# Optimization experiments

Measured on AMD Instinct MI355X. Metric: run time of the kernel, lower is better.

## Reference

```python
import jax, jax.numpy as jnp
import numpy as np

N_NODES = 50000
N_EDGES = 1600000
EMB = 128
HID = 128
OUT = 128
HEADS = 4
BN_EPS = 1e-5


def segment_softmax(e, seg, n):
    # numerically-stable softmax over variable-degree neighborhoods
    m = jax.ops.segment_max(e, seg, num_segments=n)
    m = jnp.where(jnp.isfinite(m), m, 0.0)
    ex = jnp.exp(e - m[seg])
    s = jax.ops.segment_sum(ex, seg, num_segments=n)
    return ex / (s[seg] + 1e-16)


def gat_layer(x, src, dst, W, att_src, att_dst, bias, concat):
    # PyG GATConv (eval mode, self-loops already added to src/dst)
    N = x.shape[0]
    H, C = att_src.shape
    h = (x @ W).reshape(N, H, C)                       # [N,H,C]
    a_src = jnp.einsum('nhc,hc->nh', h, att_src)       # [N,H]
    a_dst = jnp.einsum('nhc,hc->nh', h, att_dst)
    e = jax.nn.leaky_relu(a_src[src] + a_dst[dst], 0.2)  # [E,H]
    alpha = segment_softmax(e, dst, N)                 # [E,H]
    out = jax.ops.segment_sum(h[src] * alpha[:, :, None], dst, num_segments=N)
    out = out.reshape(N, H * C) if concat else out.mean(axis=1)
    return out + bias


def setup_inputs() -> dict:
    key = jax.random.key(0)
    ks = jax.random.split(key, 16)
    C1 = HID // HEADS
    inp = {
        'node_embeddings': jax.random.normal(ks[0], (N_NODES, EMB), jnp.float32),
        'edge_index': jax.random.randint(ks[1], (2, N_EDGES), 0, N_NODES, jnp.int64),
        'proj_W': jax.random.normal(ks[2], (EMB, HID), jnp.float32) * 0.05,
        'proj_b': jnp.zeros((HID,), jnp.float32),
        'W1': jax.random.normal(ks[3], (HID, HEADS * C1), jnp.float32) * 0.05,
        'att_src1': jax.random.normal(ks[4], (HEADS, C1), jnp.float32) * 0.05,
        'att_dst1': jax.random.normal(ks[5], (HEADS, C1), jnp.float32) * 0.05,
        'bias1': jnp.zeros((HEADS * C1,), jnp.float32),
        'bn_gamma': jnp.ones((HID,), jnp.float32),
        'bn_beta': jnp.zeros((HID,), jnp.float32),
        'W2': jax.random.normal(ks[6], (HID, HEADS * OUT), jnp.float32) * 0.05,
        'att_src2': jax.random.normal(ks[7], (HEADS, OUT), jnp.float32) * 0.05,
        'att_dst2': jax.random.normal(ks[8], (HEADS, OUT), jnp.float32) * 0.05,
        'bias2': jnp.zeros((OUT,), jnp.float32),
        'out_W': jax.random.normal(ks[9], (OUT, OUT), jnp.float32) * 0.05,
        'out_b': jnp.zeros((OUT,), jnp.float32),
    }
    return inp


def reference(node_embeddings, edge_index, proj_W, proj_b,
              W1, att_src1, att_dst1, bias1, bn_gamma, bn_beta,
              W2, att_src2, att_dst2, bias2, out_W, out_b):
    N = node_embeddings.shape[0]
    # add self-loops (PyG GATConv default)
    loops = jnp.arange(N, dtype=edge_index.dtype)
    src = jnp.concatenate([edge_index[0], loops])
    dst = jnp.concatenate([edge_index[1], loops])

    x = jax.nn.relu(node_embeddings @ proj_W + proj_b)
    x = gat_layer(x, src, dst, W1, att_src1, att_dst1, bias1, concat=True)
    # BatchNorm1d in eval mode: running_mean=0, running_var=1
    x = x / jnp.sqrt(1.0 + BN_EPS) * bn_gamma + bn_beta
    x = jax.nn.elu(x)
    # dropout is identity in eval mode
    x = gat_layer(x, src, dst, W2, att_src2, att_dst2, bias2, concat=False)
    x = x.mean(axis=0, keepdims=True)                  # [1, OUT]
    x = jax.nn.relu(x @ out_W + out_b)
    return x
```

## Files before the change

### kernel.cpp

```cpp
#include <hip/hip_runtime.h>
#include <hip/hip_bf16.h>

#define NN 50000
#define NROW 50048
#define NE 1600000
#define ETOT (NE + NN)
#define BN_K 0.9999950000374997f

#define SHIFT 7
#define NPB 128
#define NB ((NN + NPB - 1) >> SHIFT)
#define CAP 5120
#define CHUNK 4096
#define PGRID ((ETOT + CHUNK - 1) / CHUNK)
#define CVB (NROW * 32 / 256)

typedef __bf16 bf16x8 __attribute__((ext_vector_type(8)));
typedef float f32x4 __attribute__((ext_vector_type(4)));

__device__ __forceinline__ float leaky02(float x) { return x > 0.f ? x : 0.2f * x; }

__device__ __forceinline__ unsigned short f2bf(float f) {
    unsigned int u = __float_as_uint(f);
    u += 0x7FFFu + ((u >> 16) & 1u);
    return (unsigned short)(u >> 16);
}

__global__ void init_k(int* __restrict__ bcur_d, int* __restrict__ bcur_s,
                       float* __restrict__ y) {
    int t = threadIdx.x;
    if (t < NB) { bcur_d[t] = t * CAP; bcur_s[t] = t * CAP; }
    y[t] = 0.f;
}

__global__ void cvtw_k(const float* __restrict__ x0, unsigned short* __restrict__ x0b,
                       const float* __restrict__ pW, const float* __restrict__ W1,
                       unsigned short* __restrict__ pWt, unsigned short* __restrict__ W1t,
                       const float* __restrict__ W2, const float* __restrict__ as2,
                       const float* __restrict__ ad2, float* __restrict__ va_s,
                       float* __restrict__ va_d) {
    int b = blockIdx.x;
    if (b < CVB) {
        int g = b * 256 + threadIdx.x;
        int row = g >> 5;
        float4 v = make_float4(0.f, 0.f, 0.f, 0.f);
        if (row < NN) v = *(const float4*)&x0[(long)g * 4];
        ushort4 u;
        u.x = f2bf(v.x); u.y = f2bf(v.y); u.z = f2bf(v.z); u.w = f2bf(v.w);
        *(ushort4*)&x0b[(long)g * 4] = u;
    } else if (b < CVB + 2) {
        const float* in = (b - CVB) ? W1 : pW;
        unsigned short* outp = (b - CVB) ? W1t : pWt;
        for (int i = threadIdx.x; i < 16384; i += 256) {
            int n = i & 127, k = i >> 7;
            outp[n * 128 + k] = f2bf(in[k * 128 + n]);
        }
    } else {
        int h = b - CVB - 2;
        int k = threadIdx.x;
        if (k < 128) {
            const float* wrow = W2 + (long)k * 512 + h * 128;
            float accs = 0.f, accd = 0.f;
            for (int ci = 0; ci < 128; ++ci) {
                float w = wrow[ci];
                accs += w * as2[h * 128 + ci];
                accd += w * ad2[h * 128 + ci];
            }
            va_s[h * 128 + k] = accs;
            va_d[h * 128 + k] = accd;
        }
    }
}

__global__ __launch_bounds__(256) void fgemm_k(
    const unsigned short* __restrict__ x0b, const unsigned short* __restrict__ pWt,
    const unsigned short* __restrict__ W1t, const float* __restrict__ pb,
    const float* __restrict__ attS, const float* __restrict__ attD,
    unsigned short* __restrict__ h1b, float* __restrict__ aS, float* __restrict__ aD) {
    __shared__ unsigned short x1s[128][136];
    const int tid = threadIdx.x;
    const int wv = tid >> 6, l = tid & 63;
    const int lr = l & 15, lg = l >> 4;
    const int r0 = blockIdx.x * 128;
    const int wr = wv * 32;

    bf16x8 Af[2][4];
    f32x4 acc[2][8];

    #pragma unroll
    for (int rt = 0; rt < 2; ++rt)
        #pragma unroll
        for (int kt = 0; kt < 4; ++kt)
            Af[rt][kt] = *(const bf16x8*)&x0b[(long)(r0 + wr + rt * 16 + lr) * 128 + kt * 32 + lg * 8];
    #pragma unroll
    for (int rt = 0; rt < 2; ++rt)
        #pragma unroll
        for (int ct = 0; ct < 8; ++ct)
            acc[rt][ct] = (f32x4){0.f, 0.f, 0.f, 0.f};
    #pragma unroll
    for (int ct = 0; ct < 8; ++ct) {
        bf16x8 Bf[4];
        #pragma unroll
        for (int kt = 0; kt < 4; ++kt)
            Bf[kt] = *(const bf16x8*)&pWt[(ct * 16 + lr) * 128 + kt * 32 + lg * 8];
        #pragma unroll
        for (int kt = 0; kt < 4; ++kt) {
            acc[0][ct] = __builtin_amdgcn_mfma_f32_16x16x32_bf16(Af[0][kt], Bf[kt], acc[0][ct], 0, 0, 0);
            acc[1][ct] = __builtin_amdgcn_mfma_f32_16x16x32_bf16(Af[1][kt], Bf[kt], acc[1][ct], 0, 0, 0);
        }
    }
    #pragma unroll
    for (int ct = 0; ct < 8; ++ct) {
        int col = ct * 16 + lr;
        float bv = pb[col];
        #pragma unroll
        for (int rt = 0; rt < 2; ++rt)
            #pragma unroll
            for (int r = 0; r < 4; ++r) {
                float v = acc[rt][ct][r] + bv;
                x1s[wr + rt * 16 + lg * 4 + r][col] = f2bf(v > 0.f ? v : 0.f);
            }
    }
    __syncthreads();

    #pragma unroll
    for (int rt = 0; rt < 2; ++rt)
        #pragma unroll
        for (int kt = 0; kt < 4; ++kt)
            Af[rt][kt] = *(const bf16x8*)&x1s[wr + rt * 16 + lr][kt * 32 + lg * 8];
    #pragma unroll
    for (int rt = 0; rt < 2; ++rt)
        #pragma unroll
        for (int ct = 0; ct < 8; ++ct)
            acc[rt][ct] = (f32x4){0.f, 0.f, 0.f, 0.f};
    #pragma unroll
    for (int ct = 0; ct < 8; ++ct) {
        bf16x8 Bf[4];
        #pragma unroll
        for (int kt = 0; kt < 4; ++kt)
            Bf[kt] = *(const bf16x8*)&W1t[(ct * 16 + lr) * 128 + kt * 32 + lg * 8];
        #pragma unroll
        for (int kt = 0; kt < 4; ++kt) {
            acc[0][ct] = __builtin_amdgcn_mfma_f32_16x16x32_bf16(Af[0][kt], Bf[kt], acc[0][ct], 0, 0, 0);
            acc[1][ct] = __builtin_amdgcn_mfma_f32_16x16x32_bf16(Af[1][kt], Bf[kt], acc[1][ct], 0, 0, 0);
        }
    }
    __syncthreads();
    #pragma unroll
    for (int ct = 0; ct < 8; ++ct)
        #pragma unroll
        for (int rt = 0; rt < 2; ++rt)
            #pragma unroll
            for (int r = 0; r < 4; ++r)
                x1s[wr + rt * 16 + lg * 4 + r][ct * 16 + lr] = f2bf(acc[rt][ct][r]);
    __syncthreads();

    #pragma unroll
    for (int i = 0; i < 8; ++i) {
        int idx = tid + i * 256;
        int row = idx >> 4, cc = idx & 15;
        bf16x8 hv = *(const bf16x8*)&x1s[row][cc * 8];
        *(bf16x8*)&h1b[(long)(r0 + row) * 128 + cc * 8] = hv;
        int head = cc >> 2, lc = (cc & 3) * 8;
        float ps = 0.f, pd = 0.f;
        #pragma unroll
        for (int j = 0; j < 8; ++j) {
            float v = (float)hv[j];
            ps += v * attS[head * 32 + lc + j];
            pd += v * attD[head * 32 + lc + j];
        }
        ps += __shfl_xor(ps, 1); ps += __shfl_xor(ps, 2);
        pd += __shfl_xor(pd, 1); pd += __shfl_xor(pd, 2);
        if ((cc & 3) == 0) {
            aS[(r0 + row) * 4 + head] = ps;
            aD[(r0 + row) * 4 + head] = pd;
        }
    }
}

__global__ __launch_bounds__(512) void part_k(const int* __restrict__ srcA,
                                              const int* __restrict__ dstA,
                                              int* __restrict__ bcur_d, int* __restrict__ bcur_s,
                                              int* __restrict__ pr_d, int* __restrict__ pr_s) {
    __shared__ int cnt[NB], gb[NB], lo[NB];
    __shared__ int scanbuf[512];
    __shared__ int stg[CHUNK];
    __shared__ int dbuf[CHUNK];
    int t = threadIdx.x;
    int e0 = blockIdx.x * CHUNK;
    int e1 = min(e0 + CHUNK, ETOT);
    #pragma unroll
    for (int it = 0; it < 2; ++it) {
        int* bcur = it ? bcur_s : bcur_d;
        int* pr   = it ? pr_s   : pr_d;
        for (int i = t; i < NB; i += 512) cnt[i] = 0;
        __syncthreads();
        for (int e = e0 + t; e < e1; e += 512) {
            int s, d;
            if (e < NE) { s = srcA[e]; d = dstA[e]; } else { s = d = e - NE; }
            atomicAdd(&cnt[(it ? s : d) >> SHIFT], 1);
        }
        __syncthreads();
        for (int i = t; i < NB; i += 512)
            if (cnt[i]) gb[i] = atomicAdd(&bcur[i], cnt[i]);
        scanbuf[t] = (t < NB) ? cnt[t] : 0;
        __syncthreads();
        for (int dd = 1; dd < 512; dd <<= 1) {
            int y = (t >= dd) ? scanbuf[t - dd] : 0;
            __syncthreads();
            scanbuf[t] += y;
            __syncthreads();
        }
        if (t < NB) lo[t] = scanbuf[t] - cnt[t];
        __syncthreads();
        if (t < NB) cnt[t] = lo[t];
        __syncthreads();
        for (int e = e0 + t; e < e1; e += 512) {
            int s, d;
            if (e < NE) { s = srcA[e]; d = dstA[e]; } else { s = d = e - NE; }
            int n = it ? s : d, pay = it ? d : s;
            int key = n >> SHIFT;
            int idx = atomicAdd(&cnt[key], 1);
            stg[idx]  = ((n & (NPB - 1)) << 16) | pay;
            dbuf[idx] = gb[key] + (idx - lo[key]);
        }
        __syncthreads();
        int tot = e1 - e0;
        for (int p = t; p < tot; p += 512)
            pr[dbuf[p]] = stg[p];
        __syncthreads();
    }
}

__global__ void fine_k(const int* __restrict__ pr_d, const int* __restrict__ bcur_d,
                       int2* __restrict__ oe_d, int* __restrict__ csr_src,
                       const int* __restrict__ pr_s, const int* __restrict__ bcur_s,
                       int2* __restrict__ oe_s, int* __restrict__ csr_dst) {
    bool dk = blockIdx.x < NB;
    const int* pr    = dk ? pr_d : pr_s;
    const int* bcurb = dk ? bcur_d : bcur_s;
    int2* oe         = dk ? oe_d : oe_s;
    int* csr         = dk ? csr_src : csr_dst;
    int bkt = dk ? blockIdx.x : blockIdx.x - NB;
    __shared__ int cnt[NPB], off[NPB];
    int n0 = bkt << SHIFT;
    int base = bkt * CAP, end = bcurb[bkt];
    int t = threadIdx.x;
    if (t < NPB) cnt[t] = 0;
    __syncthreads();
    for (int i = base + t; i < end; i += 256)
        atomicAdd(&cnt[pr[i] >> 16], 1);
    __syncthreads();
    if (t < NPB) off[t] = cnt[t];
    __syncthreads();
    for (int dd = 1; dd < NPB; dd <<= 1) {
        int y = 0;
        if (t < NPB && t >= dd) y = off[t - dd];
        __syncthreads();
        if (t < NPB) off[t] += y;
        __syncthreads();
    }
    if (t < NPB) {
        int excl = off[t] - cnt[t];
        int n = n0 + t;
        if (n < NN) oe[n] = make_int2(base + excl, cnt[t]);
        off[t] = excl;
        cnt[t] = 0;
    }
    __syncthreads();
    for (int i = base + t; i < end; i += 256) {
        int p = pr[i];
        int j = p >> 16;
        int pos = base + off[j] + atomicAdd(&cnt[j], 1);
        csr[pos] = p & 0xFFFF;
    }
}

__global__ void gather1_k(const int* __restrict__ csr_src, const int2* __restrict__ oe_d,
                          const float* __restrict__ aS, const float* __restrict__ aD,
                          const unsigned short* __restrict__ h1b, const float* __restrict__ b1,
                          const float* __restrict__ bg, const float* __restrict__ bb,
                          const float* __restrict__ va_s, const float* __restrict__ va_d,
                          unsigned short* __restrict__ x2b, float* __restrict__ aS2,
                          float* __restrict__ aD2) {
    __shared__ float4 wst[4][64];
    __shared__ unsigned sst[4][64];
    int wv = threadIdx.x >> 6;
    int d = (blockIdx.x << 2) + wv;
    if (d >= NN) return;
    int lane = threadIdx.x & 63;
    float4 ad4 = *(const float4*)&aD[d * 4];
    int2 oe = oe_d[d];
    int o0 = oe.x, deg = oe.y, o1 = o0 + deg;

    float s0 = 0.f, s1 = 0.f, s2 = 0.f, s3 = 0.f;
    for (int base = o0; base < o1; base += 64) {
        int e = base + lane;
        if (e < o1) {
            int s = csr_src[e];
            float4 as4 = *(const float4*)&aS[s * 4];
            float4 w;
            w.x = __expf(leaky02(as4.x + ad4.x));
            w.y = __expf(leaky02(as4.y + ad4.y));
            w.z = __expf(leaky02(as4.z + ad4.z));
            w.w = __expf(leaky02(as4.w + ad4.w));
            wst[wv][lane] = w;
            sst[wv][lane] = (unsigned)(s << 8);
            s0 += w.x; s1 += w.y; s2 += w.z; s3 += w.w;
        }
    }
    #pragma unroll
    for (int off = 32; off; off >>= 1) {
        s0 += __shfl_xor(s0, off);
        s1 += __shfl_xor(s1, off);
        s2 += __shfl_xor(s2, off);
        s3 += __shfl_xor(s3, off);
    }
    float i0 = 1.f / (s0 + 1e-16f), i1 = 1.f / (s1 + 1e-16f);
    float i2 = 1.f / (s2 + 1e-16f), i3 = 1.f / (s3 + 1e-16f);

    int k = lane & 31, half = lane >> 5;
    unsigned cb = (unsigned)(k * 8);
    int headk = k >> 3;
    const char* h1base = (const char*)h1b;
    float a0 = 0.f, a1 = 0.f, a2 = 0.f, a3 = 0.f;

    if (deg <= 64) {
        if (lane < deg) {
            float4 w = wst[wv][lane];
            w.x *= i0; w.y *= i1; w.z *= i2; w.w *= i3;
            wst[wv][lane] = w;
        }
        __threadfence_block();
        for (int t = half; t < deg; t += 2) {
            float w = ((const float*)&wst[wv][t])[headk];
            unsigned ro = sst[wv][t];
            uint2 hv = *(const uint2*)(h1base + ro + cb);
            a0 += w * __uint_as_float(hv.x << 16);
            a1 += w * __uint_as_float(hv.x & 0xFFFF0000u);
            a2 += w * __uint_as_float(hv.y << 16);
            a3 += w * __uint_as_float(hv.y & 0xFFFF0000u);
        }
    } else {
        for (int base = o0; base < o1; base += 64) {
            int e = base + lane;
            if (e < o1) {
                int s = csr_src[e];
                float4 as4 = *(const float4*)&aS[s * 4];
                float4 w;
                w.x = __expf(leaky02(as4.x + ad4.x)) * i0;
                w.y = __expf(leaky02(as4.y + ad4.y)) * i1;
                w.z = __expf(leaky02(as4.z + ad4.z)) * i2;
                w.w = __expf(leaky02(as4.w + ad4.w)) * i3;
                wst[wv][lane] = w;
                sst[wv][lane] = (unsigned)(s << 8);
            }
            __threadfence_block();
            int nst = min(64, o1 - base);
            for (int t = half; t < nst; t += 2) {
                float w = ((const float*)&wst[wv][t])[headk];
                unsigned ro = sst[wv][t];
                uint2 hv = *(const uint2*)(h1base + ro + cb);
                a0 += w * __uint_as_float(hv.x << 16);
                a1 += w * __uint_as_float(hv.x & 0xFFFF0000u);
                a2 += w * __uint_as_float(hv.y << 16);
                a3 += w * __uint_as_float(hv.y & 0xFFFF0000u);
            }
            __threadfence_block();
        }
    }
    a0 += __shfl_xor(a0, 32); a1 += __shfl_xor(a1, 32);
    a2 += __shfl_xor(a2, 32); a3 += __shfl_xor(a3, 32);

    int c = k * 4;
    float v0 = (a0 + b1[c])     * BN_K * bg[c]     + bb[c];
    float v1 = (a1 + b1[c + 1]) * BN_K * bg[c + 1] + bb[c + 1];
    float v2 = (a2 + b1[c + 2]) * BN_K * bg[c + 2] + bb[c + 2];
    float v3 = (a3 + b1[c + 3]) * BN_K * bg[c + 3] + bb[c + 3];
    v0 = v0 > 0.f ? v0 : __expf(v0) - 1.f;
    v1 = v1 > 0.f ? v1 : __expf(v1) - 1.f;
    v2 = v2 > 0.f ? v2 : __expf(v2) - 1.f;
    v3 = v3 > 0.f ? v3 : __expf(v3) - 1.f;
    if (half == 0) {
        uint2 pk;
        pk.x = (unsigned)f2bf(v0) | ((unsigned)f2bf(v1) << 16);
        pk.y = (unsigned)f2bf(v2) | ((unsigned)f2bf(v3) << 16);
        *(uint2*)&x2b[(long)d * 128 + c] = pk;
    }

    float r[8];
    #pragma unroll
    for (int h = 0; h < 4; ++h) {
        float4 vs = *(const float4*)&va_s[h * 128 + c];
        float4 vd = *(const float4*)&va_d[h * 128 + c];
        float rs = v0 * vs.x + v1 * vs.y + v2 * vs.z + v3 * vs.w;
        float rd = v0 * vd.x + v1 * vd.y + v2 * vd.z + v3 * vd.w;
        r[h]     = half ? 0.f : rs;
        r[4 + h] = half ? 0.f : rd;
    }
    #pragma unroll
    for (int off = 32; off; off >>= 1) {
        #pragma unroll
        for (int j = 0; j < 8; ++j) r[j] += __shfl_xor(r[j], off);
    }
    if (lane == 0) {
        *(float4*)&aS2[d * 4] = make_float4(r[0], r[1], r[2], r[3]);
        *(float4*)&aD2[d * 4] = make_float4(r[4], r[5], r[6], r[7]);
    }
}

__global__ void dsum_k(const int* __restrict__ csr_src, const int2* __restrict__ oe_d,
                       const float* __restrict__ aS, const float* __restrict__ aD,
                       float* __restrict__ adL) {
    int d = (blockIdx.x << 2) + (threadIdx.x >> 6);
    if (d >= NN) return;
    int lane = threadIdx.x & 63;
    float4 ad4 = *(const float4*)&aD[d * 4];
    int2 oe = oe_d[d];
    int o0 = oe.x, o1 = oe.x + oe.y;
    float s0 = 0.f, s1 = 0.f, s2 = 0.f, s3 = 0.f;
    for (int o = o0 + lane; o < o1; o += 64) {
        int s = csr_src[o];
        float4 as4 = *(const float4*)&aS[s * 4];
        s0 += __expf(leaky02(as4.x + ad4.x));
        s1 += __expf(leaky02(as4.y + ad4.y));
        s2 += __expf(leaky02(as4.z + ad4.z));
        s3 += __expf(leaky02(as4.w + ad4.w));
    }
    #pragma unroll
    for (int off = 32; off; off >>= 1) {
        s0 += __shfl_xor(s0, off);
        s1 += __shfl_xor(s1, off);
        s2 += __shfl_xor(s2, off);
        s3 += __shfl_xor(s3, off);
    }
    if (lane == 0) {
        *(float4*)&adL[d * 8]     = ad4;
        *(float4*)&adL[d * 8 + 4] = make_float4(1.f / (s0 + 1e-16f), 1.f / (s1 + 1e-16f),
                                                1.f / (s2 + 1e-16f), 1.f / (s3 + 1e-16f));
    }
}

__global__ void waccg_k(const int* __restrict__ csr_dst, const int2* __restrict__ oe_s,
                        const float* __restrict__ aS, const float* __restrict__ adL,
                        float* __restrict__ Wacc) {
    int s = (blockIdx.x << 2) + (threadIdx.x >> 6);
    if (s >= NN) return;
    int lane = threadIdx.x & 63;
    float4 as4 = *(const float4*)&aS[s * 4];
    int2 oe = oe_s[s];
    int o0 = oe.x, o1 = oe.x + oe.y;
    float a0 = 0.f, a1 = 0.f, a2 = 0.f, a3 = 0.f;
    for (int o = o0 + lane; o < o1; o += 64) {
        int d = csr_dst[o];
        float4 ad4 = *(const float4*)&adL[d * 8];
        float4 iv  = *(const float4*)&adL[d * 8 + 4];
        a0 += __expf(leaky02(as4.x + ad4.x)) * iv.x;
        a1 += __expf(leaky02(as4.y + ad4.y)) * iv.y;
        a2 += __expf(leaky02(as4.z + ad4.z)) * iv.z;
        a3 += __expf(leaky02(as4.w + ad4.w)) * iv.w;
    }
    #pragma unroll
    for (int off = 32; off; off >>= 1) {
        a0 += __shfl_xor(a0, off);
        a1 += __shfl_xor(a1, off);
        a2 += __shfl_xor(a2, off);
        a3 += __shfl_xor(a3, off);
    }
    if (lane == 0) {
        const float scale = 0.25f / (float)NN;
        *(float4*)&Wacc[s * 4] = make_float4(scale * a0, scale * a1, scale * a2, scale * a3);
    }
}

__global__ void yacc_k(const float* __restrict__ Wacc, const unsigned short* __restrict__ x2b,
                       float* __restrict__ y) {
    int k2 = threadIdx.x;
    float a[8] = {};
    for (int r = blockIdx.x; r < NN; r += gridDim.x) {
        float4 w = *(const float4*)&Wacc[r * 4];
        unsigned hv = *(const unsigned*)&x2b[(long)r * 128 + k2 * 2];
        float xl = __uint_as_float(hv << 16);
        float xh = __uint_as_float(hv & 0xFFFF0000u);
        a[0] += w.x * xl; a[1] += w.x * xh;
        a[2] += w.y * xl; a[3] += w.y * xh;
        a[4] += w.z * xl; a[5] += w.z * xh;
        a[6] += w.w * xl; a[7] += w.w * xh;
    }
    int c = k2 * 2;
    atomicAdd(&y[0 * 128 + c], a[0]); atomicAdd(&y[0 * 128 + c + 1], a[1]);
    atomicAdd(&y[1 * 128 + c], a[2]); atomicAdd(&y[1 * 128 + c + 1], a[3]);
    atomicAdd(&y[2 * 128 + c], a[4]); atomicAdd(&y[2 * 128 + c + 1], a[5]);
    atomicAdd(&y[3 * 128 + c], a[6]); atomicAdd(&y[3 * 128 + c + 1], a[7]);
}

__global__ void final2_k(const float* __restrict__ y, const float* __restrict__ W2,
                         const float* __restrict__ b2, const float* __restrict__ oW,
                         const float* __restrict__ ob, float* __restrict__ out) {
    __shared__ float xm[128];
    int c = threadIdx.x;
    float t = b2[c];
    #pragma unroll
    for (int h = 0; h < 4; ++h) {
        const float* yh = y + h * 128;
        for (int k = 0; k < 128; ++k) t += yh[k] * W2[(long)k * 512 + h * 128 + c];
    }
    xm[c] = t;
    __syncthreads();
    float acc = ob[c];
    for (int k = 0; k < 128; ++k) acc += xm[k] * oW[k * 128 + c];
    out[c] = acc > 0.f ? acc : 0.f;
}

extern "C" void kernel_launch(void* const* d_in, const int* in_sizes, int n_in,
                              void* d_out, int out_size, void* d_ws, size_t ws_size,
                              hipStream_t stream) {
    const float* x0  = (const float*)d_in[0];
    const int*   ei  = (const int*)d_in[1];
    const float* pW  = (const float*)d_in[2];
    const float* pb  = (const float*)d_in[3];
    const float* W1  = (const float*)d_in[4];
    const float* as1 = (const float*)d_in[5];
    const float* ad1 = (const float*)d_in[6];
    const float* b1  = (const float*)d_in[7];
    const float* bg  = (const float*)d_in[8];
    const float* bb  = (const float*)d_in[9];
    const float* W2  = (const float*)d_in[10];
    const float* as2 = (const float*)d_in[11];
    const float* ad2 = (const float*)d_in[12];
    const float* b2  = (const float*)d_in[13];
    const float* oW  = (const float*)d_in[14];
    const float* ob  = (const float*)d_in[15];
    float* out = (float*)d_out;

    float* ws = (float*)d_ws;
    unsigned short* x0b = (unsigned short*)ws; ws += 3203072;
    unsigned short* h1b = (unsigned short*)ws; ws += 3203072;
    unsigned short* x2b = (unsigned short*)ws; ws += 3200000;
    unsigned short* pWt = (unsigned short*)ws; ws += 8192;
    unsigned short* W1t = (unsigned short*)ws; ws += 8192;
    float* aS1   = ws; ws += 200192;
    float* aD1   = ws; ws += 200192;
    float* aS2   = ws; ws += 200000;
    float* aD2   = ws; ws += 200000;
    float* adL   = ws; ws += 400000;
    float* Wacc  = ws; ws += 200000;
    float* va_s  = ws; ws += 512;
    float* va_d  = ws; ws += 512;
    float* y     = ws; ws += 512;
    int* bcur_d  = (int*)ws; ws += NB;
    int* bcur_s  = (int*)ws; ws += NB;
    int2* oe_d   = (int2*)ws; ws += 2 * NN;
    int2* oe_s   = (int2*)ws; ws += 2 * NN;
    int* csr_src = (int*)ws; ws += NB * CAP;
    int* csr_dst = (int*)ws; ws += NB * CAP;
    int* pr_d    = (int*)ws; ws += NB * CAP;
    int* pr_s    = (int*)ws; ws += NB * CAP;

    const int* srcA = ei;
    const int* dstA = ei + NE;

    dim3 blk(256);

    init_k<<<1, 512, 0, stream>>>(bcur_d, bcur_s, y);
    cvtw_k<<<CVB + 6, blk, 0, stream>>>(x0, x0b, pW, W1, pWt, W1t, W2, as2, ad2, va_s, va_d);
    part_k<<<PGRID, 512, 0, stream>>>(srcA, dstA, bcur_d, bcur_s, pr_d, pr_s);
    fine_k<<<2 * NB, blk, 0, stream>>>(pr_d, bcur_d, oe_d, csr_src,
                                       pr_s, bcur_s, oe_s, csr_dst);

    fgemm_k<<<NB, blk, 0, stream>>>(x0b, pWt, W1t, pb, as1, ad1, h1b, aS1, aD1);

    gather1_k<<<12500, blk, 0, stream>>>(csr_src, oe_d, aS1, aD1, h1b, b1, bg, bb,
                                         va_s, va_d, x2b, aS2, aD2);

    dsum_k<<<12500, blk, 0, stream>>>(csr_src, oe_d, aS2, aD2, adL);
    waccg_k<<<12500, blk, 0, stream>>>(csr_dst, oe_s, aS2, adL, Wacc);
    yacc_k<<<256, 64, 0, stream>>>(Wacc, x2b, y);
    final2_k<<<1, 128, 0, stream>>>(y, W2, b2, oW, ob, out);
}
```

Baseline: 396.8 us.

## Fuse input bf16 conversion into GEMM, merge partition passes, fold init kernel

New measurement: 378.7 us. 4.6% less time.

```diff
diff --git a/kernel.cpp b/kernel.cpp
--- a/kernel.cpp
+++ b/kernel.cpp
@@ -2,7 +2,6 @@
 #include <hip/hip_bf16.h>
 
 #define NN 50000
-#define NROW 50048
 #define NE 1600000
 #define ETOT (NE + NN)
 #define BN_K 0.9999950000374997f
@@ -11,9 +10,8 @@
 #define NPB 128
 #define NB ((NN + NPB - 1) >> SHIFT)
 #define CAP 5120
-#define CHUNK 4096
+#define CHUNK 3072
 #define PGRID ((ETOT + CHUNK - 1) / CHUNK)
-#define CVB (NROW * 32 / 256)
 
 typedef __bf16 bf16x8 __attribute__((ext_vector_type(8)));
 typedef float f32x4 __attribute__((ext_vector_type(4)));
@@ -26,54 +24,42 @@
     return (unsigned short)(u >> 16);
 }
 
-__global__ void init_k(int* __restrict__ bcur_d, int* __restrict__ bcur_s,
-                       float* __restrict__ y) {
-    int t = threadIdx.x;
-    if (t < NB) { bcur_d[t] = t * CAP; bcur_s[t] = t * CAP; }
-    y[t] = 0.f;
-}
-
-__global__ void cvtw_k(const float* __restrict__ x0, unsigned short* __restrict__ x0b,
-                       const float* __restrict__ pW, const float* __restrict__ W1,
+__global__ void prep_k(const float* __restrict__ pW, const float* __restrict__ W1,
                        unsigned short* __restrict__ pWt, unsigned short* __restrict__ W1t,
                        const float* __restrict__ W2, const float* __restrict__ as2,
                        const float* __restrict__ ad2, float* __restrict__ va_s,
-                       float* __restrict__ va_d) {
+                       float* __restrict__ va_d, int* __restrict__ bcur_d,
+                       int* __restrict__ bcur_s, float* __restrict__ y) {
     int b = blockIdx.x;
-    if (b < CVB) {
-        int g = b * 256 + threadIdx.x;
-        int row = g >> 5;
-        float4 v = make_float4(0.f, 0.f, 0.f, 0.f);
-        if (row < NN) v = *(const float4*)&x0[(long)g * 4];
-        ushort4 u;
-        u.x = f2bf(v.x); u.y = f2bf(v.y); u.z = f2bf(v.z); u.w = f2bf(v.w);
-        *(ushort4*)&x0b[(long)g * 4] = u;
-    } else if (b < CVB + 2) {
-        const float* in = (b - CVB) ? W1 : pW;
-        unsigned short* outp = (b - CVB) ? W1t : pWt;
-        for (int i = threadIdx.x; i < 16384; i += 256) {
+    int t = threadIdx.x;
+    if (b < 2) {
+        const float* in = b ? W1 : pW;
+        unsigned short* outp = b ? W1t : pWt;
+        for (int i = t; i < 16384; i += 256) {
             int n = i & 127, k = i >> 7;
             outp[n * 128 + k] = f2bf(in[k * 128 + n]);
         }
-    } else {
-        int h = b - CVB - 2;
-        int k = threadIdx.x;
-        if (k < 128) {
-            const float* wrow = W2 + (long)k * 512 + h * 128;
+    } else if (b < 6) {
+        int h = b - 2;
+        if (t < 128) {
+            const float* wrow = W2 + (long)t * 512 + h * 128;
             float accs = 0.f, accd = 0.f;
             for (int ci = 0; ci < 128; ++ci) {
                 float w = wrow[ci];
                 accs += w * as2[h * 128 + ci];
                 accd += w * ad2[h * 128 + ci];
             }
-            va_s[h * 128 + k] = accs;
-            va_d[h * 128 + k] = accd;
-        }
+            va_s[h * 128 + t] = accs;
+            va_d[h * 128 + t] = accd;
+        }
+    } else {
+        for (int i = t; i < NB; i += 256) { bcur_d[i] = i * CAP; bcur_s[i] = i * CAP; }
+        for (int i = t; i < 512; i += 256) y[i] = 0.f;
     }
 }
 
 __global__ __launch_bounds__(256) void fgemm_k(
-    const unsigned short* __restrict__ x0b, const unsigned short* __restrict__ pWt,
+    const float* __restrict__ x0, const unsigned short* __restrict__ pWt,
     const unsigned short* __restrict__ W1t, const float* __restrict__ pb,
     const float* __restrict__ attS, const float* __restrict__ attD,
     unsigned short* __restrict__ h1b, float* __restrict__ aS, float* __restrict__ aD) {
@@ -88,10 +74,24 @@
     f32x4 acc[2][8];
 
     #pragma unroll
-    for (int rt = 0; rt < 2; ++rt)
-        #pragma unroll
-        for (int kt = 0; kt < 4; ++kt)
-            Af[rt][kt] = *(const bf16x8*)&x0b[(long)(r0 + wr + rt * 16 + lr) * 128 + kt * 32 + lg * 8];
+    for (int rt = 0; rt < 2; ++rt) {
+        int row = r0 + wr + rt * 16 + lr;
+        #pragma unroll
+        for (int kt = 0; kt < 4; ++kt) {
+            bf16x8 a;
+            if (row < NN) {
+                const float* p = &x0[(long)row * 128 + kt * 32 + lg * 8];
+                float4 v0 = *(const float4*)p;
+                float4 v1 = *(const float4*)(p + 4);
+                a[0] = (__bf16)v0.x; a[1] = (__bf16)v0.y; a[2] = (__bf16)v0.z; a[3] = (__bf16)v0.w;
+                a[4] = (__bf16)v1.x; a[5] = (__bf16)v1.y; a[6] = (__bf16)v1.z; a[7] = (__bf16)v1.w;
+            } else {
+                #pragma unroll
+                for (int j = 0; j < 8; ++j) a[j] = (__bf16)0.f;
+            }
+            Af[rt][kt] = a;
+        }
+    }
     #pragma unroll
     for (int rt = 0; rt < 2; ++rt)
         #pragma unroll
@@ -182,60 +182,72 @@
                                               const int* __restrict__ dstA,
                                               int* __restrict__ bcur_d, int* __restrict__ bcur_s,
                                               int* __restrict__ pr_d, int* __restrict__ pr_s) {
-    __shared__ int cnt[NB], gb[NB], lo[NB];
+    __shared__ int cd[NB], cs[NB], gbd[NB], gbs[NB], lod[NB], los[NB];
     __shared__ int scanbuf[512];
-    __shared__ int stg[CHUNK];
-    __shared__ int dbuf[CHUNK];
+    __shared__ int stg_d[CHUNK], db_d[CHUNK], stg_s[CHUNK], db_s[CHUNK];
     int t = threadIdx.x;
     int e0 = blockIdx.x * CHUNK;
     int e1 = min(e0 + CHUNK, ETOT);
-    #pragma unroll
-    for (int it = 0; it < 2; ++it) {
-        int* bcur = it ? bcur_s : bcur_d;
-        int* pr   = it ? pr_s   : pr_d;
-        for (int i = t; i < NB; i += 512) cnt[i] = 0;
+    for (int i = t; i < NB; i += 512) { cd[i] = 0; cs[i] = 0; }
+    __syncthreads();
+    for (int e = e0 + t; e < e1; e += 512) {
+        int s, d;
+        if (e < NE) { s = srcA[e]; d = dstA[e]; } else { s = d = e - NE; }
+        atomicAdd(&cd[d >> SHIFT], 1);
+        atomicAdd(&cs[s >> SHIFT], 1);
+    }
+    __syncthreads();
+    for (int i = t; i < NB; i += 512) {
+        if (cd[i]) gbd[i] = atomicAdd(&bcur_d[i], cd[i]);
+        if (cs[i]) gbs[i] = atomicAdd(&bcur_s[i], cs[i]);
+    }
+    scanbuf[t] = (t < NB) ? cd[t] : 0;
+    __syncthreads();
+    for (int dd = 1; dd < 512; dd <<= 1) {
+        int yv = (t >= dd) ? scanbuf[t - dd] : 0;
         __syncthreads();
-        for (int e = e0 + t; e < e1; e += 512) {
-            int s, d;
-            if (e < NE) { s = srcA[e]; d = dstA[e]; } else { s = d = e - NE; }
-            atomicAdd(&cnt[(it ? s : d) >> SHIFT], 1);
-        }
+        scanbuf[t] += yv;
         __syncthreads();
-        for (int i = t; i < NB; i += 512)
-            if (cnt[i]) gb[i] = atomicAdd(&bcur[i], cnt[i]);
-        scanbuf[t] = (t < NB) ? cnt[t] : 0;
+    }
+    if (t < NB) lod[t] = scanbuf[t] - cd[t];
+    __syncthreads();
+    scanbuf[t] = (t < NB) ? cs[t] : 0;
+    __syncthreads();
+    for (int dd = 1; dd < 512; dd <<= 1) {
+        int yv = (t >= dd) ? scanbuf[t - dd] : 0;
         __syncthreads();
-        for (int dd = 1; dd < 512; dd <<= 1) {
-            int y = (t >= dd) ? scanbuf[t - dd] : 0;
-            __syncthreads();
-            scanbuf[t] += y;
-            __syncthreads();
-        }
-        if (t < NB) lo[t] = scanbuf[t] - cnt[t];
+        scanbuf[t] += yv;
         __syncthreads();
-        if (t < NB) cnt[t] = lo[t];
-        __syncthreads();
-        for (int e = e0 + t; e < e1; e += 512) {
-            int s, d;
-            if (e < NE) { s = srcA[e]; d = dstA[e]; } else { s = d = e - NE; }
-            int n = it ? s : d, pay = it ? d : s;
-            int key = n >> SHIFT;
-            int idx = atomicAdd(&cnt[key], 1);
-            stg[idx]  = ((n & (NPB - 1)) << 16) | pay;
-            dbuf[idx] = gb[key] + (idx - lo[key]);
-        }
-        __syncthreads();
-        int tot = e1 - e0;
-        for (int p = t; p < tot; p += 512)
-            pr[dbuf[p]] = stg[p];
-        __syncthreads();
-    }
-}
-
-__global__ void fine_k(const int* __restrict__ pr_d, const int* __restrict__ bcur_d,
-                       int2* __restrict__ oe_d, int* __restrict__ csr_src,
-                       const int* __restrict__ pr_s, const int* __restrict__ bcur_s,
-                       int2* __restrict__ oe_s, int* __restrict__ csr_dst) {
+    }
+    if (t < NB) los[t] = scanbuf[t] - cs[t];
+    __syncthreads();
+    if (t < NB) { cd[t] = lod[t]; cs[t] = los[t]; }
+    __syncthreads();
+    for (int e = e0 + t; e < e1; e += 512) {
+        int s, d;
+        if (e < NE) { s = srcA[e]; d = dstA[e]; } else { s = d = e - NE; }
+        int kd = d >> SHIFT;
+        int id = atomicAdd(&cd[kd], 1);
+        stg_d[id] = ((d & (NPB - 1)) << 16) | s;
+        db_d[id]  = gbd[kd] + (id - lod[kd]);
+        int ks = s >> SHIFT;
+        int is = atomicAdd(&cs[ks], 1);
+        stg_s[is] = ((s & (NPB - 1)) << 16) | d;
+        db_s[is]  = gbs[ks] + (is - los[ks]);
+    }
+    __syncthreads();
+    int tot = e1 - e0;
+    for (int p = t; p < tot; p += 512) {
+        pr_d[db_d[p]] = stg_d[p];
+        pr_s[db_s[p]] = stg_s[p];
+    }
+}
+
+__global__ __launch_bounds__(512) void fine_k(
+        const int* __restrict__ pr_d, const int* __restrict__ bcur_d,
+        int2* __restrict__ oe_d, int* __restrict__ csr_src,
+        const int* __restrict__ pr_s, const int* __restrict__ bcur_s,
+        int2* __restrict__ oe_s, int* __restrict__ csr_dst) {
     bool dk = blockIdx.x < NB;
     const int* pr    = dk ? pr_d : pr_s;
     const int* bcurb = dk ? bcur_d : bcur_s;
@@ -248,16 +260,16 @@
     int t = threadIdx.x;
     if (t < NPB) cnt[t] = 0;
     __syncthreads();
-    for (int i = base + t; i < end; i += 256)
+    for (int i = base + t; i < end; i += 512)
         atomicAdd(&cnt[pr[i] >> 16], 1);
     __syncthreads();
     if (t < NPB) off[t] = cnt[t];
     __syncthreads();
     for (int dd = 1; dd < NPB; dd <<= 1) {
-        int y = 0;
-        if (t < NPB && t >= dd) y = off[t - dd];
+        int yv = 0;
+        if (t < NPB && t >= dd) yv = off[t - dd];
         __syncthreads();
-        if (t < NPB) off[t] += y;
+        if (t < NPB) off[t] += yv;
         __syncthreads();
     }
     if (t < NPB) {
@@ -268,7 +280,7 @@
         cnt[t] = 0;
     }
     __syncthreads();
-    for (int i = base + t; i < end; i += 256) {
+    for (int i = base + t; i < end; i += 512) {
         int p = pr[i];
         int j = p >> 16;
         int pos = base + off[j] + atomicAdd(&cnt[j], 1);
@@ -534,7 +546,6 @@
     float* out = (float*)d_out;
 
     float* ws = (float*)d_ws;
-    unsigned short* x0b = (unsigned short*)ws; ws += 3203072;
     unsigned short* h1b = (unsigned short*)ws; ws += 3203072;
     unsigned short* x2b = (unsigned short*)ws; ws += 3200000;
     unsigned short* pWt = (unsigned short*)ws; ws += 8192;
@@ -562,19 +573,19 @@
 
     dim3 blk(256);
 
-    init_k<<<1, 512, 0, stream>>>(bcur_d, bcur_s, y);
-    cvtw_k<<<CVB + 6, blk, 0, stream>>>(x0, x0b, pW, W1, pWt, W1t, W2, as2, ad2, va_s, va_d);
+    prep_k<<<7, blk, 0, stream>>>(pW, W1, pWt, W1t, W2, as2, ad2, va_s, va_d,
+                                  bcur_d, bcur_s, y);
     part_k<<<PGRID, 512, 0, stream>>>(srcA, dstA, bcur_d, bcur_s, pr_d, pr_s);
-    fine_k<<<2 * NB, blk, 0, stream>>>(pr_d, bcur_d, oe_d, csr_src,
+    fine_k<<<2 * NB, 512, 0, stream>>>(pr_d, bcur_d, oe_d, csr_src,
                                        pr_s, bcur_s, oe_s, csr_dst);
 
-    fgemm_k<<<NB, blk, 0, stream>>>(x0b, pWt, W1t, pb, as1, ad1, h1b, aS1, aD1);
+    fgemm_k<<<NB, blk, 0, stream>>>(x0, pWt, W1t, pb, as1, ad1, h1b, aS1, aD1);
 
     gather1_k<<<12500, blk, 0, stream>>>(csr_src, oe_d, aS1, aD1, h1b, b1, bg, bb,
                                          va_s, va_d, x2b, aS2, aD2);
 
     dsum_k<<<12500, blk, 0, stream>>>(csr_src, oe_d, aS2, aD2, adL);
     waccg_k<<<12500, blk, 0, stream>>>(csr_dst, oe_s, aS2, adL, Wacc);
-    yacc_k<<<256, 64, 0, stream>>>(Wacc, x2b, y);
+    yacc_k<<<512, 64, 0, stream>>>(Wacc, x2b, y);
     final2_k<<<1, 128, 0, stream>>>(y, W2, b2, oW, ob, out);
 }
```
